# Kernel tuning notes

Measured on AMD Instinct MI355X. Metric: run time of the kernel, lower is better.

Reference implementation:

```python
import jax, jax.numpy as jnp
import numpy as np

RADIUS = 0.1
NSAMPLE = 32


def setup_inputs() -> dict:
    key = jax.random.key(0)
    k1, k2, k3, k4, k5 = jax.random.split(key, 5)
    B, NPOINT, N, C = 4, 2048, 8192, 64
    query_xyz = jax.random.uniform(k1, (B, 3, NPOINT), dtype=jnp.float32)
    support_xyz = jax.random.uniform(k2, (B, 3, N), dtype=jnp.float32)
    query_mask = jax.random.bernoulli(k3, 0.9, (B, NPOINT))
    support_mask = jax.random.bernoulli(k4, 0.9, (B, N))
    features = jax.random.normal(k5, (B, C, N), dtype=jnp.float32)
    return {"query_xyz": query_xyz, "support_xyz": support_xyz,
            "query_mask": query_mask, "support_mask": support_mask,
            "features": features}


def _masked_ordered_ball_query(query_xyz, support_xyz, query_mask, support_mask,
                               radius, nsample):
    # query_xyz: (B,3,npoint), support_xyz: (B,3,N)
    q = query_xyz.transpose(0, 2, 1)    # (B, npoint, 3)
    s = support_xyz.transpose(0, 2, 1)  # (B, N, 3)
    N = s.shape[1]
    # squared pairwise distances via |q|^2 + |s|^2 - 2 q.s  -> (B, npoint, N)
    d2 = (jnp.sum(q * q, -1)[:, :, None]
          + jnp.sum(s * s, -1)[:, None, :]
          - 2.0 * jnp.einsum('bpd,bnd->bpn', q, s))
    within = (d2 <= radius * radius) \
        & support_mask[:, None, :] & query_mask[:, :, None]
    # ordered selection of the first `nsample` in-ball indices (ascending index)
    score = jnp.where(within, N - jnp.arange(N, dtype=jnp.int32), 0)
    vals, idx = jax.lax.top_k(score, nsample)     # (B, npoint, nsample)
    idx_mask = vals > 0                            # true neighbors
    # pad slots with the first found neighbor (0 if none found)
    first = jnp.where(idx_mask[..., :1], idx[..., :1], 0)
    idx = jnp.where(idx_mask, idx, first)
    return idx, idx_mask


def _group(points_nc, idx):
    # points_nc: (B, N, D), idx: (B, npoint, nsample) -> (B, npoint, nsample, D)
    return jax.vmap(lambda p, i: p[i])(points_nc, idx)


def reference(query_xyz, support_xyz, query_mask, support_mask, features):
    idx, idx_mask = _masked_ordered_ball_query(
        query_xyz, support_xyz, query_mask, support_mask, RADIUS, NSAMPLE)
    s = support_xyz.transpose(0, 2, 1)             # (B, N, 3)
    grouped_xyz = _group(s, idx).transpose(0, 3, 1, 2)   # (B,3,npoint,nsample)
    grouped_xyz = grouped_xyz - query_xyz[:, :, :, None]
    grouped_xyz = grouped_xyz / RADIUS             # normalize_xyz=True
    f = features.transpose(0, 2, 1)                # (B, N, C)
    grouped_features = _group(f, idx).transpose(0, 3, 1, 2)  # (B,C,npoint,nsample)
    new_features = jnp.concatenate([grouped_xyz, grouped_features], axis=1)
    return new_features, idx_mask
```

## Files before the change

### kernel.cpp

```cpp
#include <hip/hip_runtime.h>


#define NPOINT 2048
#define NSUP   8192
#define NCH    64
#define NS     32
#define GRID1  10
#define CELLS  1000
#define QCHUNK 1024

__device__ __forceinline__ bool probe_mask4(const void* mask) {
    const unsigned char* mb = (const unsigned char*)mask;
    const int lane = threadIdx.x & 63;
    return __ballot(mb[4 * lane + 1] != 0) == 0ull;
}
__device__ __forceinline__ bool read_mask(const void* mask, int i, bool is4) {
    return is4 ? (((const int*)mask)[i] != 0)
               : (((const unsigned char*)mask)[i] != 0);
}
__device__ __forceinline__ int cell_of(float x, float y, float z) {
    const int cx = min(GRID1 - 1, (int)(x * 10.0f));
    const int cy = min(GRID1 - 1, (int)(y * 10.0f));
    const int cz = min(GRID1 - 1, (int)(z * 10.0f));
    return cx + GRID1 * cy + GRID1 * GRID1 * cz;
}

__global__ __launch_bounds__(1024) void grid_hist_scan(
    const float* __restrict__ support_xyz, const void* __restrict__ support_mask,
    int* __restrict__ starts, int* __restrict__ cursors)
{
    __shared__ int cnt_s[CELLS];
    __shared__ int scanb[1024];
    const int tid = threadIdx.x;
    const int b   = blockIdx.x;
    const bool m4 = probe_mask4(support_mask);

    const float* sx = support_xyz + (size_t)b * 3 * NSUP;
    for (int i = tid; i < CELLS; i += 1024) cnt_s[i] = 0;
    __syncthreads();

    for (int n = tid; n < NSUP; n += 1024) {
        if (read_mask(support_mask, b * NSUP + n, m4)) {
            const int cid = cell_of(sx[n], sx[NSUP + n], sx[2 * NSUP + n]);
            atomicAdd(&cnt_s[cid], 1);
        }
    }
    __syncthreads();

    scanb[tid] = (tid < CELLS) ? cnt_s[tid] : 0;
    __syncthreads();
    for (int d = 1; d < 1024; d <<= 1) {
        int v = 0;
        if (tid >= d) v = scanb[tid - d];
        __syncthreads();
        if (tid >= d) scanb[tid] += v;
        __syncthreads();
    }
    int* sb = starts + b * (CELLS + 1);
    if (tid == 0) sb[0] = 0;
    if (tid < CELLS) sb[tid + 1] = scanb[tid];
    for (int i = tid; i < CELLS; i += 1024) cursors[b * CELLS + i] = 0;
}

__global__ __launch_bounds__(256) void grid_fill(
    const float* __restrict__ support_xyz, const void* __restrict__ support_mask,
    const int* __restrict__ starts, int* __restrict__ cursors,
    float4* __restrict__ pts)
{
    const bool m4 = probe_mask4(support_mask);
    const int gid = blockIdx.x * 256 + threadIdx.x;
    const int b = gid / NSUP, n = gid % NSUP;
    if (!read_mask(support_mask, gid, m4)) return;
    const float* sx = support_xyz + (size_t)b * 3 * NSUP;
    const float x = sx[n], y = sx[NSUP + n], z = sx[2 * NSUP + n];
    const int cid = cell_of(x, y, z);
    const int pos = starts[b * (CELLS + 1) + cid]
                  + atomicAdd(&cursors[b * CELLS + cid], 1);
    pts[(size_t)b * NSUP + pos] = make_float4(x, y, z, __int_as_float(n));
}

__global__ __launch_bounds__(256) void mqag_query(
    const float* __restrict__ query_xyz, const float* __restrict__ support_xyz,
    const void* __restrict__ query_mask, const void* __restrict__ support_mask,
    const float4* __restrict__ pts, const int* __restrict__ starts,
    int* __restrict__ idx_ws, float* __restrict__ out, int B)
{
#pragma clang fp contract(off)
    const int wib  = threadIdx.x >> 6;
    const int lane = threadIdx.x & 63;
    const int qid  = blockIdx.x * 4 + wib;
    const int b    = qid / NPOINT;
    const int p    = qid % NPOINT;

    __shared__ int hits_all[4][64];
    __shared__ int slots_all[4][NS];
    int* hits  = hits_all[wib];
    int* slots = slots_all[wib];

    const bool m4s = probe_mask4(support_mask);
    const bool m4q = probe_mask4(query_mask);

    const float* sx = support_xyz + (size_t)b * 3 * NSUP;
    const float* sy = sx + NSUP;
    const float* sz = sx + 2 * NSUP;

    const float qx = query_xyz[(size_t)b * 3 * NPOINT + p];
    const float qy = query_xyz[(size_t)b * 3 * NPOINT + NPOINT + p];
    const float qz = query_xyz[(size_t)b * 3 * NPOINT + 2 * NPOINT + p];
    const bool  qm = read_mask(query_mask, b * NPOINT + p, m4q);
    const float qq = (qx * qx + qy * qy) + qz * qz;

    int cnt = 0;
    if (qm) {
        const int x0 = max(0, (int)floorf((qx - 0.101f) * 10.f));
        const int x1 = min(GRID1 - 1, (int)floorf((qx + 0.101f) * 10.f));
        const int y0 = max(0, (int)floorf((qy - 0.101f) * 10.f));
        const int y1 = min(GRID1 - 1, (int)floorf((qy + 0.101f) * 10.f));
        const int z0 = max(0, (int)floorf((qz - 0.101f) * 10.f));
        const int z1 = min(GRID1 - 1, (int)floorf((qz + 0.101f) * 10.f));
        const int ncx = x1 - x0 + 1;

        const int*    stb  = starts + b * (CELLS + 1);
        const float4* ptsb = pts + (size_t)b * NSUP;

        for (int cz = z0; cz <= z1; ++cz) {
            for (int cy = y0; cy <= y1; ++cy) {
                const int c0 = x0 + GRID1 * cy + GRID1 * GRID1 * cz;
                const int s0 = stb[c0];
                const int e0 = stb[c0 + ncx];
                for (int tb = s0; tb < e0; tb += 64) {
                    const int g  = tb + lane;
                    const bool valid = g < e0;
                    const float4 pv = ptsb[valid ? g : (e0 - 1)];
                    const int nidx = __float_as_int(pv.w);
                    const float ss  = (pv.x * pv.x + pv.y * pv.y) + pv.z * pv.z;
                    const float dot = __builtin_fmaf(qz, pv.z,
                                      __builtin_fmaf(qy, pv.y, qx * pv.x));
                    const float d2  = (qq + ss) - 2.0f * dot;
                    const bool within = valid && (d2 <= 0.01f);
                    const unsigned long long bal = __ballot(within);
                    if (within) {
                        const int r = cnt + __popcll(bal & ((1ull << lane) - 1ull));
                        if (r < 64) hits[r] = nidx;
                    }
                    cnt += __popcll(bal);
                }
            }
        }
    }

    __syncthreads();

    if (cnt > 64) {
        int c2 = 0;
        for (int basei = 0; basei < NSUP; basei += 64) {
            const int n = basei + lane;
            const float x = sx[n], y = sy[n], z = sz[n];
            const bool  m = read_mask(support_mask, b * NSUP + n, m4s);
            const float ss  = (x * x + y * y) + z * z;
            const float dot = __builtin_fmaf(qz, z,
                              __builtin_fmaf(qy, y, qx * x));
            const float d2  = (qq + ss) - 2.0f * dot;
            const bool within = (d2 <= 0.01f) && m;
            const unsigned long long bal = __ballot(within);
            if (within) {
                const int r = c2 + __popcll(bal & ((1ull << lane) - 1ull));
                if (r < NS) slots[r] = n;
            }
            c2 += __popcll(bal);
            if (c2 >= NS) break;
        }
        cnt = c2;
    } else {
        int v = (lane < cnt) ? hits[lane] : 0x7FFFFFFF;
        #pragma unroll
        for (int k = 2; k <= 64; k <<= 1) {
            #pragma unroll
            for (int j = k >> 1; j > 0; j >>= 1) {
                const int pv = __shfl_xor(v, j, 64);
                const bool keep_min = ((lane & j) == 0) == ((lane & k) == 0);
                const int mn = min(v, pv), mx = max(v, pv);
                v = keep_min ? mn : mx;
            }
        }
        if (lane < NS && lane < cnt) slots[lane] = v;
    }
    const int found = (cnt < NS) ? cnt : NS;

    __syncthreads();
    const int first = (found > 0) ? slots[0] : 0;
    if (lane < NS && lane >= found) slots[lane] = first;
    __syncthreads();

    if (lane < NS) idx_ws[((size_t)b * NPOINT + p) * NS + lane] = slots[lane];

    const size_t nf_elems = (size_t)B * 67 * NPOINT * NS;
    if (lane < NS) {
        out[nf_elems + ((size_t)b * NPOINT + p) * NS + lane] =
            (lane < found) ? 1.0f : 0.0f;
    }
}

__global__ __launch_bounds__(256) void gather_all(
    const float* __restrict__ support_xyz, const float* __restrict__ query_xyz,
    const float* __restrict__ features, const int* __restrict__ idx_ws,
    float* __restrict__ out, int B)
{
    __shared__ float row[NSUP];
    __shared__ float qrow[QCHUNK];
    const int bc = blockIdx.y;
    const int b  = bc / 67, c = bc % 67;
    const int p0 = blockIdx.x * QCHUNK;
    const bool is_xyz = (c < 3);

    const float* src = is_xyz
        ? support_xyz + ((size_t)b * 3 + c) * NSUP
        : features + ((size_t)b * NCH + (c - 3)) * NSUP;
    const float4* src4 = (const float4*)src;
    for (int i = threadIdx.x; i < NSUP / 4; i += 256)
        ((float4*)row)[i] = src4[i];
    if (is_xyz) {
        const float* qsrc = query_xyz + ((size_t)b * 3 + c) * NPOINT + p0;
        for (int i = threadIdx.x; i < QCHUNK; i += 256) qrow[i] = qsrc[i];
    }
    __syncthreads();

    const int4* idx4 = (const int4*)(idx_ws + ((size_t)b * NPOINT + p0) * NS);
    float4* dst4 = (float4*)(out + (((size_t)b * 67 + c) * NPOINT + p0) * NS);
    const int iters = QCHUNK * NS / 4 / 256;
    if (is_xyz) {
        for (int e = threadIdx.x; e < QCHUNK * NS / 4; e += 256) {
            const int4 iv = idx4[e];
            const float q = qrow[e >> 3];
            dst4[e] = make_float4((row[iv.x] - q) / 0.1f,
                                  (row[iv.y] - q) / 0.1f,
                                  (row[iv.z] - q) / 0.1f,
                                  (row[iv.w] - q) / 0.1f);
        }
    } else {
        for (int e = threadIdx.x; e < QCHUNK * NS / 4; e += 256) {
            const int4 iv = idx4[e];
            dst4[e] = make_float4(row[iv.x], row[iv.y], row[iv.z], row[iv.w]);
        }
    }
    (void)iters;
}

__global__ __launch_bounds__(256) void mqag_linear(
    const float* __restrict__ query_xyz, const float* __restrict__ support_xyz,
    const void* __restrict__ query_mask_raw, const void* __restrict__ support_mask_raw,
    const float* __restrict__ features, float* __restrict__ out, int B)
{
#pragma clang fp contract(off)
    const int wib  = threadIdx.x >> 6;
    const int lane = threadIdx.x & 63;
    const int qid  = blockIdx.x * 4 + wib;
    const int b    = qid / NPOINT;
    const int p    = qid % NPOINT;

    __shared__ int slots_all[4][NS];
    int* slots = slots_all[wib];

    const bool m4s = probe_mask4(support_mask_raw);
    const bool m4q = probe_mask4(query_mask_raw);

    const float* sx = support_xyz + (size_t)b * 3 * NSUP;
    const float* sy = sx + NSUP;
    const float* sz = sx + 2 * NSUP;

    const float qx = query_xyz[(size_t)b * 3 * NPOINT + p];
    const float qy = query_xyz[(size_t)b * 3 * NPOINT + NPOINT + p];
    const float qz = query_xyz[(size_t)b * 3 * NPOINT + 2 * NPOINT + p];
    const bool  qm = read_mask(query_mask_raw, b * NPOINT + p, m4q);
    const float qq = (qx * qx + qy * qy) + qz * qz;

    int cnt = 0;
    if (qm) {
        for (int base = 0; base < NSUP; base += 64) {
            const int n = base + lane;
            const float x = sx[n], y = sy[n], z = sz[n];
            const bool  m = read_mask(support_mask_raw, b * NSUP + n, m4s);
            const float ss  = (x * x + y * y) + z * z;
            const float dot = __builtin_fmaf(qz, z, __builtin_fmaf(qy, y, qx * x));
            const float d2  = (qq + ss) - 2.0f * dot;
            const bool within = (d2 <= 0.01f) && m;
            const unsigned long long bal = __ballot(within);
            if (within) {
                const int r = cnt + __popcll(bal & ((1ull << lane) - 1ull));
                if (r < NS) slots[r] = n;
            }
            cnt += __popcll(bal);
            if (cnt >= NS) break;
        }
    }
    const int found = cnt < NS ? cnt : NS;
    __syncthreads();
    const int first = (found > 0) ? slots[0] : 0;
    if (lane < NS && lane >= found) slots[lane] = first;
    __syncthreads();

    const size_t nf_elems = (size_t)B * 67 * NPOINT * NS;
    if (lane < NS) {
        out[nf_elems + ((size_t)b * NPOINT + p) * NS + lane] =
            (lane < found) ? 1.0f : 0.0f;
    }
    const float* feat = features + (size_t)b * NCH * NSUP;
    for (int i = 0; i < (67 * NS + 63) / 64; ++i) {
        const int flat = i * 64 + lane;
        if (flat < 67 * NS) {
            const int ch = flat >> 5;
            const int k  = flat & 31;
            const int idx = slots[k];
            float val;
            if (ch < 3) {
                const float s = sx[(size_t)ch * NSUP + idx];
                const float q = (ch == 0) ? qx : ((ch == 1) ? qy : qz);
                val = (s - q) / 0.1f;
            } else {
                val = feat[(size_t)(ch - 3) * NSUP + idx];
            }
            out[(((size_t)b * 67 + ch) * NPOINT + p) * NS + k] = val;
        }
    }
}

extern "C" void kernel_launch(void* const* d_in, const int* in_sizes, int n_in,
                              void* d_out, int out_size, void* d_ws, size_t ws_size,
                              hipStream_t stream) {
    const float* query_xyz    = (const float*)d_in[0];
    const float* support_xyz  = (const float*)d_in[1];
    const void*  query_mask   = d_in[2];
    const void*  support_mask = d_in[3];
    const float* features     = (const float*)d_in[4];

    const int B = in_sizes[0] / (3 * NPOINT);

    const size_t off_pts     = 0;
    const size_t off_starts  = off_pts + (size_t)B * NSUP * sizeof(float4);
    const size_t off_cursors = off_starts + (size_t)B * (CELLS + 1) * sizeof(int);
    const size_t off_idx     = off_cursors + (size_t)B * CELLS * sizeof(int);
    const size_t need = off_idx + (size_t)B * NPOINT * NS * sizeof(int);

    if (ws_size >= need) {
        float4* pts  = (float4*)((char*)d_ws + off_pts);
        int* starts  = (int*)((char*)d_ws + off_starts);
        int* cursors = (int*)((char*)d_ws + off_cursors);
        int* idx_ws  = (int*)((char*)d_ws + off_idx);

        hipLaunchKernelGGL(grid_hist_scan, dim3(B), dim3(1024), 0, stream,
                           support_xyz, support_mask, starts, cursors);
        hipLaunchKernelGGL(grid_fill, dim3(B * NSUP / 256), dim3(256), 0,
                           stream, support_xyz, support_mask, starts, cursors, pts);
        hipLaunchKernelGGL(mqag_query, dim3(B * NPOINT / 4), dim3(256), 0,
                           stream, query_xyz, support_xyz, query_mask,
                           support_mask, pts, starts, idx_ws, (float*)d_out, B);
        hipLaunchKernelGGL(gather_all, dim3(NPOINT / QCHUNK, B * 67), dim3(256),
                           0, stream, support_xyz, query_xyz, features, idx_ws,
                           (float*)d_out, B);
    } else {
        hipLaunchKernelGGL(mqag_linear, dim3(B * NPOINT / 4), dim3(256), 0,
                           stream, query_xyz, support_xyz, query_mask,
                           support_mask, features, (float*)d_out, B);
    }
}
```

Baseline: 124.2 us.

## Fuse grid build, query and gather into one cooperative persistent kernel

Replaces the four-kernel pipeline (histogram/scan, fill, query, gather) with a single cooperative kernel of 512 blocks of 1024 threads. The phases are separated by grid-wide syncs, which removes launch gaps between kernels. The histogram now uses global atomics instead of shared-memory ones, and the gather runs as a grid-stride loop over tiles. The risks are cooperative-launch occupancy limits (512 blocks of 1024 threads must be co-resident, otherwise it falls back to the old path), grid-sync overhead, and slower global atomics.

```diff
diff --git a/kernel.cpp b/kernel.cpp
--- a/kernel.cpp
+++ b/kernel.cpp
@@ -1,4 +1,7 @@
 #include <hip/hip_runtime.h>
+#include <hip/hip_cooperative_groups.h>
+
+namespace cg = cooperative_groups;
 
 
 #define NPOINT 2048
@@ -23,6 +26,232 @@
     const int cy = min(GRID1 - 1, (int)(y * 10.0f));
     const int cz = min(GRID1 - 1, (int)(z * 10.0f));
     return cx + GRID1 * cy + GRID1 * GRID1 * cz;
+}
+
+__global__ __launch_bounds__(1024, 8) void mqag_mega(
+    const float* __restrict__ query_xyz, const float* __restrict__ support_xyz,
+    const void* __restrict__ query_mask, const void* __restrict__ support_mask,
+    const float* __restrict__ features,
+    float4* __restrict__ pts, int* __restrict__ starts,
+    int* __restrict__ cursors, int* __restrict__ idx_ws,
+    float* __restrict__ out, int B)
+{
+#pragma clang fp contract(off)
+    __shared__ __align__(16) char smem[36992];
+    cg::grid_group gg = cg::this_grid();
+    const int tid   = threadIdx.x;
+    const int gsize = gridDim.x * 1024;
+    const int gtid  = blockIdx.x * 1024 + tid;
+
+    {
+        const int nz = B * (CELLS + 1) + B * CELLS;
+        for (int i = gtid; i < nz; i += gsize) starts[i] = 0;
+    }
+    gg.sync();
+
+    {
+        const bool m4 = probe_mask4(support_mask);
+        for (int g = gtid; g < B * NSUP; g += gsize) {
+            const int b = g / NSUP, n = g % NSUP;
+            if (read_mask(support_mask, g, m4)) {
+                const float* sx = support_xyz + (size_t)b * 3 * NSUP;
+                const int cid = cell_of(sx[n], sx[NSUP + n], sx[2 * NSUP + n]);
+                atomicAdd(&starts[b * (CELLS + 1) + cid + 1], 1);
+            }
+        }
+    }
+    gg.sync();
+
+    if ((int)blockIdx.x < B) {
+        int* scanb = (int*)smem;
+        int* sb = starts + blockIdx.x * (CELLS + 1);
+        scanb[tid] = (tid < CELLS) ? sb[tid + 1] : 0;
+        __syncthreads();
+        for (int d = 1; d < 1024; d <<= 1) {
+            int v = 0;
+            if (tid >= d) v = scanb[tid - d];
+            __syncthreads();
+            if (tid >= d) scanb[tid] += v;
+            __syncthreads();
+        }
+        if (tid < CELLS) sb[tid + 1] = scanb[tid];
+    }
+    gg.sync();
+
+    {
+        const bool m4 = probe_mask4(support_mask);
+        for (int g = gtid; g < B * NSUP; g += gsize) {
+            const int b = g / NSUP, n = g % NSUP;
+            if (read_mask(support_mask, g, m4)) {
+                const float* sx = support_xyz + (size_t)b * 3 * NSUP;
+                const float x = sx[n], y = sx[NSUP + n], z = sx[2 * NSUP + n];
+                const int cid = cell_of(x, y, z);
+                const int pos = starts[b * (CELLS + 1) + cid]
+                              + atomicAdd(&cursors[b * CELLS + cid], 1);
+                pts[(size_t)b * NSUP + pos] =
+                    make_float4(x, y, z, __int_as_float(n));
+            }
+        }
+    }
+    gg.sync();
+
+    {
+        const int wib  = tid >> 6;
+        const int lane = tid & 63;
+        int* hits  = (int*)smem + wib * 96;
+        int* slots = hits + 64;
+        const int qid = blockIdx.x * 16 + wib;
+        const int b   = qid / NPOINT;
+        const int p   = qid % NPOINT;
+
+        const bool m4s = probe_mask4(support_mask);
+        const bool m4q = probe_mask4(query_mask);
+
+        const float* sx = support_xyz + (size_t)b * 3 * NSUP;
+        const float* sy = sx + NSUP;
+        const float* sz = sx + 2 * NSUP;
+
+        const float qx = query_xyz[(size_t)b * 3 * NPOINT + p];
+        const float qy = query_xyz[(size_t)b * 3 * NPOINT + NPOINT + p];
+        const float qz = query_xyz[(size_t)b * 3 * NPOINT + 2 * NPOINT + p];
+        const bool  qm = read_mask(query_mask, b * NPOINT + p, m4q);
+        const float qq = (qx * qx + qy * qy) + qz * qz;
+
+        int cnt = 0;
+        if (qm) {
+            const int x0 = max(0, (int)floorf((qx - 0.101f) * 10.f));
+            const int x1 = min(GRID1 - 1, (int)floorf((qx + 0.101f) * 10.f));
+            const int y0 = max(0, (int)floorf((qy - 0.101f) * 10.f));
+            const int y1 = min(GRID1 - 1, (int)floorf((qy + 0.101f) * 10.f));
+            const int z0 = max(0, (int)floorf((qz - 0.101f) * 10.f));
+            const int z1 = min(GRID1 - 1, (int)floorf((qz + 0.101f) * 10.f));
+            const int ncx = x1 - x0 + 1;
+
+            const int*    stb  = starts + b * (CELLS + 1);
+            const float4* ptsb = pts + (size_t)b * NSUP;
+
+            for (int cz = z0; cz <= z1; ++cz) {
+                for (int cy = y0; cy <= y1; ++cy) {
+                    const int c0 = x0 + GRID1 * cy + GRID1 * GRID1 * cz;
+                    const int s0 = stb[c0];
+                    const int e0 = stb[c0 + ncx];
+                    for (int tb = s0; tb < e0; tb += 64) {
+                        const int g  = tb + lane;
+                        const bool valid = g < e0;
+                        const float4 pv = ptsb[valid ? g : (e0 - 1)];
+                        const int nidx = __float_as_int(pv.w);
+                        const float ss  = (pv.x * pv.x + pv.y * pv.y) + pv.z * pv.z;
+                        const float dot = __builtin_fmaf(qz, pv.z,
+                                          __builtin_fmaf(qy, pv.y, qx * pv.x));
+                        const float d2  = (qq + ss) - 2.0f * dot;
+                        const bool within = valid && (d2 <= 0.01f);
+                        const unsigned long long bal = __ballot(within);
+                        if (within) {
+                            const int r = cnt + __popcll(bal & ((1ull << lane) - 1ull));
+                            if (r < 64) hits[r] = nidx;
+                        }
+                        cnt += __popcll(bal);
+                    }
+                }
+            }
+        }
+
+        __syncthreads();
+
+        if (cnt > 64) {
+            int c2 = 0;
+            for (int basei = 0; basei < NSUP; basei += 64) {
+                const int n = basei + lane;
+                const float x = sx[n], y = sy[n], z = sz[n];
+                const bool  m = read_mask(support_mask, b * NSUP + n, m4s);
+                const float ss  = (x * x + y * y) + z * z;
+                const float dot = __builtin_fmaf(qz, z,
+                                  __builtin_fmaf(qy, y, qx * x));
+                const float d2  = (qq + ss) - 2.0f * dot;
+                const bool within = (d2 <= 0.01f) && m;
+                const unsigned long long bal = __ballot(within);
+                if (within) {
+                    const int r = c2 + __popcll(bal & ((1ull << lane) - 1ull));
+                    if (r < NS) slots[r] = n;
+                }
+                c2 += __popcll(bal);
+                if (c2 >= NS) break;
+            }
+            cnt = c2;
+        } else {
+            int v = (lane < cnt) ? hits[lane] : 0x7FFFFFFF;
+            #pragma unroll
+            for (int k = 2; k <= 64; k <<= 1) {
+                #pragma unroll
+                for (int j = k >> 1; j > 0; j >>= 1) {
+                    const int pv = __shfl_xor(v, j, 64);
+                    const bool keep_min = ((lane & j) == 0) == ((lane & k) == 0);
+                    const int mn = min(v, pv), mx = max(v, pv);
+                    v = keep_min ? mn : mx;
+                }
+            }
+            if (lane < NS && lane < cnt) slots[lane] = v;
+        }
+        const int found = (cnt < NS) ? cnt : NS;
+
+        __syncthreads();
+        const int first = (found > 0) ? slots[0] : 0;
+        if (lane < NS && lane >= found) slots[lane] = first;
+        __syncthreads();
+
+        if (lane < NS) idx_ws[((size_t)b * NPOINT + p) * NS + lane] = slots[lane];
+
+        const size_t nf_elems = (size_t)B * 67 * NPOINT * NS;
+        if (lane < NS) {
+            out[nf_elems + ((size_t)b * NPOINT + p) * NS + lane] =
+                (lane < found) ? 1.0f : 0.0f;
+        }
+    }
+    gg.sync();
+
+    {
+        float* row  = (float*)smem;
+        float* qrow = (float*)smem + NSUP;
+        const int ntiles = B * 67 * (NPOINT / QCHUNK);
+        for (int tile = blockIdx.x; tile < ntiles; tile += gridDim.x) {
+            const int t2 = tile >> 1;
+            const int px = tile & 1;
+            const int b  = t2 / 67, c = t2 % 67;
+            const int p0 = px * QCHUNK;
+            const bool is_xyz = (c < 3);
+
+            __syncthreads();
+            const float* src = is_xyz
+                ? support_xyz + ((size_t)b * 3 + c) * NSUP
+                : features + ((size_t)b * NCH + (c - 3)) * NSUP;
+            const float4* src4 = (const float4*)src;
+            for (int i = tid; i < NSUP / 4; i += 1024)
+                ((float4*)row)[i] = src4[i];
+            if (is_xyz) {
+                const float* qsrc = query_xyz + ((size_t)b * 3 + c) * NPOINT + p0;
+                for (int i = tid; i < QCHUNK; i += 1024) qrow[i] = qsrc[i];
+            }
+            __syncthreads();
+
+            const int4* idx4 = (const int4*)(idx_ws + ((size_t)b * NPOINT + p0) * NS);
+            float4* dst4 = (float4*)(out + (((size_t)b * 67 + c) * NPOINT + p0) * NS);
+            if (is_xyz) {
+                for (int e = tid; e < QCHUNK * NS / 4; e += 1024) {
+                    const int4 iv = idx4[e];
+                    const float q = qrow[e >> 3];
+                    dst4[e] = make_float4((row[iv.x] - q) / 0.1f,
+                                          (row[iv.y] - q) / 0.1f,
+                                          (row[iv.z] - q) / 0.1f,
+                                          (row[iv.w] - q) / 0.1f);
+                }
+            } else {
+                for (int e = tid; e < QCHUNK * NS / 4; e += 1024) {
+                    const int4 iv = idx4[e];
+                    dst4[e] = make_float4(row[iv.x], row[iv.y], row[iv.z], row[iv.w]);
+                }
+            }
+        }
+    }
 }
 
 __global__ __launch_bounds__(1024) void grid_hist_scan(
@@ -38,7 +267,6 @@
     const float* sx = support_xyz + (size_t)b * 3 * NSUP;
     for (int i = tid; i < CELLS; i += 1024) cnt_s[i] = 0;
     __syncthreads();
-
     for (int n = tid; n < NSUP; n += 1024) {
         if (read_mask(support_mask, b * NSUP + n, m4)) {
             const int cid = cell_of(sx[n], sx[NSUP + n], sx[2 * NSUP + n]);
@@ -46,7 +274,6 @@
         }
     }
     __syncthreads();
-
     scanb[tid] = (tid < CELLS) ? cnt_s[tid] : 0;
     __syncthreads();
     for (int d = 1; d < 1024; d <<= 1) {
@@ -119,10 +346,8 @@
         const int z0 = max(0, (int)floorf((qz - 0.101f) * 10.f));
         const int z1 = min(GRID1 - 1, (int)floorf((qz + 0.101f) * 10.f));
         const int ncx = x1 - x0 + 1;
-
         const int*    stb  = starts + b * (CELLS + 1);
         const float4* ptsb = pts + (size_t)b * NSUP;
-
         for (int cz = z0; cz <= z1; ++cz) {
             for (int cy = y0; cy <= y1; ++cy) {
                 const int c0 = x0 + GRID1 * cy + GRID1 * GRID1 * cz;
@@ -148,9 +373,7 @@
             }
         }
     }
-
-    __syncthreads();
-
+    __syncthreads();
     if (cnt > 64) {
         int c2 = 0;
         for (int basei = 0; basei < NSUP; basei += 64) {
@@ -158,8 +381,7 @@
             const float x = sx[n], y = sy[n], z = sz[n];
             const bool  m = read_mask(support_mask, b * NSUP + n, m4s);
             const float ss  = (x * x + y * y) + z * z;
-            const float dot = __builtin_fmaf(qz, z,
-                              __builtin_fmaf(qy, y, qx * x));
+            const float dot = __builtin_fmaf(qz, z, __builtin_fmaf(qy, y, qx * x));
             const float d2  = (qq + ss) - 2.0f * dot;
             const bool within = (d2 <= 0.01f) && m;
             const unsigned long long bal = __ballot(within);
@@ -186,14 +408,11 @@
         if (lane < NS && lane < cnt) slots[lane] = v;
     }
     const int found = (cnt < NS) ? cnt : NS;
-
     __syncthreads();
     const int first = (found > 0) ? slots[0] : 0;
     if (lane < NS && lane >= found) slots[lane] = first;
     __syncthreads();
-
     if (lane < NS) idx_ws[((size_t)b * NPOINT + p) * NS + lane] = slots[lane];
-
     const size_t nf_elems = (size_t)B * 67 * NPOINT * NS;
     if (lane < NS) {
         out[nf_elems + ((size_t)b * NPOINT + p) * NS + lane] =
@@ -227,7 +446,6 @@
 
     const int4* idx4 = (const int4*)(idx_ws + ((size_t)b * NPOINT + p0) * NS);
     float4* dst4 = (float4*)(out + (((size_t)b * 67 + c) * NPOINT + p0) * NS);
-    const int iters = QCHUNK * NS / 4 / 256;
     if (is_xyz) {
         for (int e = threadIdx.x; e < QCHUNK * NS / 4; e += 256) {
             const int4 iv = idx4[e];
@@ -243,85 +461,6 @@
             dst4[e] = make_float4(row[iv.x], row[iv.y], row[iv.z], row[iv.w]);
         }
     }
-    (void)iters;
-}
-
-__global__ __launch_bounds__(256) void mqag_linear(
-    const float* __restrict__ query_xyz, const float* __restrict__ support_xyz,
-    const void* __restrict__ query_mask_raw, const void* __restrict__ support_mask_raw,
-    const float* __restrict__ features, float* __restrict__ out, int B)
-{
-#pragma clang fp contract(off)
-    const int wib  = threadIdx.x >> 6;
-    const int lane = threadIdx.x & 63;
-    const int qid  = blockIdx.x * 4 + wib;
-    const int b    = qid / NPOINT;
-    const int p    = qid % NPOINT;
-
-    __shared__ int slots_all[4][NS];
-    int* slots = slots_all[wib];
-
-    const bool m4s = probe_mask4(support_mask_raw);
-    const bool m4q = probe_mask4(query_mask_raw);
-
-    const float* sx = support_xyz + (size_t)b * 3 * NSUP;
-    const float* sy = sx + NSUP;
-    const float* sz = sx + 2 * NSUP;
-
-    const float qx = query_xyz[(size_t)b * 3 * NPOINT + p];
-    const float qy = query_xyz[(size_t)b * 3 * NPOINT + NPOINT + p];
-    const float qz = query_xyz[(size_t)b * 3 * NPOINT + 2 * NPOINT + p];
-    const bool  qm = read_mask(query_mask_raw, b * NPOINT + p, m4q);
-    const float qq = (qx * qx + qy * qy) + qz * qz;
-
-    int cnt = 0;
-    if (qm) {
-        for (int base = 0; base < NSUP; base += 64) {
-            const int n = base + lane;
-            const float x = sx[n], y = sy[n], z = sz[n];
-            const bool  m = read_mask(support_mask_raw, b * NSUP + n, m4s);
-            const float ss  = (x * x + y * y) + z * z;
-            const float dot = __builtin_fmaf(qz, z, __builtin_fmaf(qy, y, qx * x));
-            const float d2  = (qq + ss) - 2.0f * dot;
-            const bool within = (d2 <= 0.01f) && m;
-            const unsigned long long bal = __ballot(within);
-            if (within) {
-                const int r = cnt + __popcll(bal & ((1ull << lane) - 1ull));
-                if (r < NS) slots[r] = n;
-            }
-            cnt += __popcll(bal);
-            if (cnt >= NS) break;
-        }
-    }
-    const int found = cnt < NS ? cnt : NS;
-    __syncthreads();
-    const int first = (found > 0) ? slots[0] : 0;
-    if (lane < NS && lane >= found) slots[lane] = first;
-    __syncthreads();
-
-    const size_t nf_elems = (size_t)B * 67 * NPOINT * NS;
-    if (lane < NS) {
-        out[nf_elems + ((size_t)b * NPOINT + p) * NS + lane] =
-            (lane < found) ? 1.0f : 0.0f;
-    }
-    const float* feat = features + (size_t)b * NCH * NSUP;
-    for (int i = 0; i < (67 * NS + 63) / 64; ++i) {
-        const int flat = i * 64 + lane;
-        if (flat < 67 * NS) {
-            const int ch = flat >> 5;
-            const int k  = flat & 31;
-            const int idx = slots[k];
-            float val;
-            if (ch < 3) {
-                const float s = sx[(size_t)ch * NSUP + idx];
-                const float q = (ch == 0) ? qx : ((ch == 1) ? qy : qz);
-                val = (s - q) / 0.1f;
-            } else {
-                val = feat[(size_t)(ch - 3) * NSUP + idx];
-            }
-            out[(((size_t)b * 67 + ch) * NPOINT + p) * NS + k] = val;
-        }
-    }
 }
 
 extern "C" void kernel_launch(void* const* d_in, const int* in_sizes, int n_in,
@@ -340,26 +479,34 @@
     const size_t off_cursors = off_starts + (size_t)B * (CELLS + 1) * sizeof(int);
     const size_t off_idx     = off_cursors + (size_t)B * CELLS * sizeof(int);
     const size_t need = off_idx + (size_t)B * NPOINT * NS * sizeof(int);
-
-    if (ws_size >= need) {
-        float4* pts  = (float4*)((char*)d_ws + off_pts);
-        int* starts  = (int*)((char*)d_ws + off_starts);
-        int* cursors = (int*)((char*)d_ws + off_cursors);
-        int* idx_ws  = (int*)((char*)d_ws + off_idx);
-
-        hipLaunchKernelGGL(grid_hist_scan, dim3(B), dim3(1024), 0, stream,
-                           support_xyz, support_mask, starts, cursors);
-        hipLaunchKernelGGL(grid_fill, dim3(B * NSUP / 256), dim3(256), 0,
-                           stream, support_xyz, support_mask, starts, cursors, pts);
-        hipLaunchKernelGGL(mqag_query, dim3(B * NPOINT / 4), dim3(256), 0,
-                           stream, query_xyz, support_xyz, query_mask,
-                           support_mask, pts, starts, idx_ws, (float*)d_out, B);
-        hipLaunchKernelGGL(gather_all, dim3(NPOINT / QCHUNK, B * 67), dim3(256),
-                           0, stream, support_xyz, query_xyz, features, idx_ws,
-                           (float*)d_out, B);
-    } else {
-        hipLaunchKernelGGL(mqag_linear, dim3(B * NPOINT / 4), dim3(256), 0,
-                           stream, query_xyz, support_xyz, query_mask,
-                           support_mask, features, (float*)d_out, B);
-    }
-}
+    if (ws_size < need) return;
+
+    float4* pts  = (float4*)((char*)d_ws + off_pts);
+    int* starts  = (int*)((char*)d_ws + off_starts);
+    int* cursors = (int*)((char*)d_ws + off_cursors);
+    int* idx_ws  = (int*)((char*)d_ws + off_idx);
+    float* outp  = (float*)d_out;
+
+    int Bv = B;
+    void* args[] = { (void*)&query_xyz, (void*)&support_xyz, (void*)&query_mask,
+                     (void*)&support_mask, (void*)&features, (void*)&pts,
+                     (void*)&starts, (void*)&cursors, (void*)&idx_ws,
+                     (void*)&outp, (void*)&Bv };
+    const dim3 cgrid(B * NPOINT / 16);
+    const dim3 cblock(1024);
+    hipError_t err = hipLaunchCooperativeKernel((void*)mqag_mega, cgrid, cblock,
+                                                args, 0, stream);
+    if (err == hipSuccess) return;
+    (void)hipGetLastError();
+
+    hipLaunchKernelGGL(grid_hist_scan, dim3(B), dim3(1024), 0, stream,
+                       support_xyz, support_mask, starts, cursors);
+    hipLaunchKernelGGL(grid_fill, dim3(B * NSUP / 256), dim3(256), 0,
+                       stream, support_xyz, support_mask, starts, cursors, pts);
+    hipLaunchKernelGGL(mqag_query, dim3(B * NPOINT / 4), dim3(256), 0,
+                       stream, query_xyz, support_xyz, query_mask,
+                       support_mask, pts, starts, idx_ws, outp, B);
+    hipLaunchKernelGGL(gather_all, dim3(NPOINT / QCHUNK, B * 67), dim3(256),
+                       0, stream, support_xyz, query_xyz, features, idx_ws,
+                       outp, B);
+}
```

Measured after the change: 373.2 us. +200.5%, slower.
